# Kernel optimization log

Measured on AMD Instinct MI355X. Metric: run time of the kernel, lower is better.

## Reference

```python
import jax, jax.numpy as jnp
import numpy as np

NUM_HEADS = 16
HEAD_DIM = 64
HIDDEN = NUM_HEADS * HEAD_DIM


def _rotate_half(x):
    half = x.shape[-1] // 2
    x1, x2 = x[..., :half], x[..., half:]
    return jnp.concatenate([-x2, x1], axis=-1)


def setup_inputs() -> dict:
    key = jax.random.key(0)
    k1, k2, k3, k4, k5 = jax.random.split(key, 5)
    B, T = 2, 2048
    x = jax.random.normal(k1, (B, T, HIDDEN), dtype=jnp.float32)
    # rotary tables (seq_len, head_dim) as in apply_rope docstring
    cos = jax.random.uniform(k2, (T, HEAD_DIM), dtype=jnp.float32)
    sin = jax.random.uniform(k3, (T, HEAD_DIM), dtype=jnp.float32)
    # nn.Linear weights: y = x @ W.T ; scaled for stable fp32 activations
    w_qkv = jax.random.normal(k4, (3 * HIDDEN, HIDDEN), dtype=jnp.float32) * (1.0 / np.sqrt(HIDDEN))
    w_out = jax.random.normal(k5, (HIDDEN, HIDDEN), dtype=jnp.float32) * (1.0 / np.sqrt(HIDDEN))
    return {"x": x, "cos": cos, "sin": sin, "w_qkv": w_qkv, "w_out": w_out}


def reference(x, cos, sin, w_qkv, w_out):
    B, T, C = x.shape
    H, D = NUM_HEADS, HEAD_DIM
    qkv = jnp.einsum("btc,fc->btf", x, w_qkv)          # (B, T, 3C)
    q, k, v = jnp.split(qkv, 3, axis=-1)
    # (B, T, C) -> (B, H, T, D)
    to_heads = lambda t: t.reshape(B, T, H, D).transpose(0, 2, 1, 3)
    q, k, v = to_heads(q), to_heads(k), to_heads(v)
    # RoPE: broadcast cos/sin (T, D) over batch and heads
    cos_b = cos[None, None, :, :]
    sin_b = sin[None, None, :, :]
    q = q * cos_b + _rotate_half(q) * sin_b
    k = k * cos_b + _rotate_half(k) * sin_b
    # causal scaled dot-product attention (dropout_p = 0 in eval)
    scale = 1.0 / np.sqrt(D)
    scores = jnp.einsum("bhqd,bhkd->bhqk", q, k) * scale  # (B, H, T, T)
    causal = jnp.tril(jnp.ones((T, T), dtype=bool))
    scores = jnp.where(causal[None, None], scores, jnp.finfo(scores.dtype).min)
    probs = jax.nn.softmax(scores, axis=-1)
    out = jnp.einsum("bhqk,bhkd->bhqd", probs, v)          # (B, H, T, D)
    out = out.transpose(0, 2, 1, 3).reshape(B, T, C)
    return jnp.einsum("btc,fc->btf", out, w_out)
```

## Files before the change

kernel.cpp:

```cpp
#include <hip/hip_runtime.h>

typedef unsigned short u16;
typedef __bf16 bf16x8 __attribute__((ext_vector_type(8)));
typedef __bf16 bf16x4 __attribute__((ext_vector_type(4)));
typedef float f32x4 __attribute__((ext_vector_type(4)));

__device__ __forceinline__ u16 f2bf(float f) {
    union { float f; unsigned int i; } v; v.f = f;
    unsigned int x = v.i;
    x += 0x7fffu + ((x >> 16) & 1u);
    return (u16)(x >> 16);
}

__device__ __forceinline__ void gl_lds16(const u16* g, u16* l) {
    __builtin_amdgcn_global_load_lds(
        (const __attribute__((address_space(1))) void*)g,
        (__attribute__((address_space(3))) void*)l, 16, 0, 0);
}

__global__ __launch_bounds__(256, 2)
void cvt_xw_kernel(const float* __restrict__ X, const float* __restrict__ Wq,
                   u16* __restrict__ Xb, u16* __restrict__ Wqb)
{
    const int n1 = 4194304 / 4;
    const int n2 = 3145728 / 4;
    int i = blockIdx.x * 256 + threadIdx.x;
    const int stride = gridDim.x * 256;
    for (; i < n1 + n2; i += stride) {
        float4 v;
        ushort4* dst;
        if (i < n1) { v = ((const float4*)X)[i];       dst = (ushort4*)Xb + i; }
        else        { v = ((const float4*)Wq)[i - n1]; dst = (ushort4*)Wqb + (i - n1); }
        ushort4 o;
        o.x = f2bf(v.x); o.y = f2bf(v.y); o.z = f2bf(v.z); o.w = f2bf(v.w);
        *dst = o;
    }
}

__global__ __launch_bounds__(256, 2)
void cvt_w_kernel(const float* __restrict__ W, u16* __restrict__ Wb)
{
    int i = blockIdx.x * 256 + threadIdx.x;
    float4 v = ((const float4*)W)[i];
    ushort4 o;
    o.x = f2bf(v.x); o.y = f2bf(v.y); o.z = f2bf(v.z); o.w = f2bf(v.w);
    ((ushort4*)Wb)[i] = o;
}

__global__ __launch_bounds__(256, 2)
void qkv_rope_kernel(const u16* __restrict__ X, const u16* __restrict__ W,
                     const float* __restrict__ Cos, const float* __restrict__ Sin,
                     u16* __restrict__ Qo, u16* __restrict__ Ko, u16* __restrict__ Vo)
{
    __shared__ __align__(16) u16 As[128 * 64];
    __shared__ __align__(16) u16 Bs[128 * 64];
    const int tid  = threadIdx.x;
    const int lane = tid & 63, wave = tid >> 6;
    const int l15  = lane & 15, q4 = lane >> 4;
    const int wm = (wave >> 1) * 64, wn = (wave & 1) * 64;
    const int m0 = blockIdx.y * 128, n0 = blockIdx.x * 128;
    const int srow = lane >> 3;
    const int scol = ((lane & 7) ^ srow) * 8;

    f32x4 acc[4][4];
    #pragma unroll
    for (int i = 0; i < 4; i++)
        #pragma unroll
        for (int j = 0; j < 4; j++) { f32x4 z = {}; acc[i][j] = z; }

    for (int k0 = 0; k0 < 1024; k0 += 64) {
        __syncthreads();
        #pragma unroll
        for (int i = 0; i < 4; i++) {
            int rb = wave * 32 + i * 8;
            gl_lds16(X + (size_t)(m0 + rb + srow) * 1024 + k0 + scol, As + rb * 64);
            gl_lds16(W + (size_t)(n0 + rb + srow) * 1024 + k0 + scol, Bs + rb * 64);
        }
        __syncthreads();
        #pragma unroll
        for (int ks = 0; ks < 2; ks++) {
            const int ch = (((4 * ks + q4) ^ (l15 & 7)) * 8);
            bf16x8 af[4], bfr[4];
            #pragma unroll
            for (int i = 0; i < 4; i++) {
                af[i]  = *(const bf16x8*)&As[(wm + i * 16 + l15) * 64 + ch];
                bfr[i] = *(const bf16x8*)&Bs[(wn + i * 16 + l15) * 64 + ch];
            }
            #pragma unroll
            for (int mi = 0; mi < 4; mi++)
                #pragma unroll
                for (int ni = 0; ni < 4; ni++)
                    acc[mi][ni] = __builtin_amdgcn_mfma_f32_16x16x32_bf16(
                        af[mi], bfr[ni], acc[mi][ni], 0, 0, 0);
        }
    }

    if (n0 >= 2048) {
        #pragma unroll
        for (int mi = 0; mi < 4; mi++) {
            int t0row = m0 + wm + mi * 16 + q4 * 4;
            int b = t0row >> 11, t0 = t0row & 2047;
            #pragma unroll
            for (int ni = 0; ni < 4; ni++) {
                int col = n0 + wn + ni * 16 + l15;
                int hh  = (col >> 6) & 15;
                int d   = col & 63;
                ushort4 pk;
                pk.x = f2bf(acc[mi][ni][0]); pk.y = f2bf(acc[mi][ni][1]);
                pk.z = f2bf(acc[mi][ni][2]); pk.w = f2bf(acc[mi][ni][3]);
                *(ushort4*)&Vo[(((size_t)(b * 16 + hh)) * 64 + d) * 2048 + t0] = pk;
            }
        }
    } else {
        #pragma unroll
        for (int mi = 0; mi < 4; mi++) {
            #pragma unroll
            for (int r = 0; r < 4; r++) {
                int row = m0 + wm + mi * 16 + q4 * 4 + r;
                int b = row >> 11, t = row & 2047;
                #pragma unroll
                for (int ni = 0; ni < 4; ni++) {
                    int col = n0 + wn + ni * 16 + l15;
                    float v = acc[mi][ni][r];
                    int sec = col >> 10;
                    int hh  = (col >> 6) & 15;
                    int d   = col & 63;
                    float cs = Cos[t * 64 + d];
                    float sn = Sin[t * 64 + d];
                    float partner = acc[mi][ni ^ 2][r];
                    float rot = (d < 32) ? -partner : partner;
                    v = v * cs + rot * sn;
                    u16* dst = (sec == 0) ? Qo : Ko;
                    dst[(((size_t)(b * 16 + hh)) * 2048 + t) * 64 + d] = f2bf(v);
                }
            }
        }
    }
}

__global__ __launch_bounds__(256, 3)
void attn_kernel(const u16* __restrict__ Q, const u16* __restrict__ Kg,
                 const u16* __restrict__ Vt, u16* __restrict__ Oh)
{
    __shared__ __align__(16) u16 Ks[128 * 64];
    __shared__ __align__(16) u16 Vs[64 * 128];
    __shared__ __align__(16) __bf16 Ps[4][16][136];

    const int bx = blockIdx.x;
    const int xcd = bx & 7;
    const int i8  = bx >> 3;
    const int bh  = xcd * 4 + (i8 & 3);
    const int qt  = 31 - (i8 >> 2);
    const int b = bh >> 4, h = bh & 15;
    const int tid = threadIdx.x, wave = tid >> 6, lane = tid & 63;
    const int l15 = lane & 15, q4 = lane >> 4;
    const int srow = lane >> 3;
    const int sKcol = ((lane & 7) ^ srow) * 8;

    const size_t head_off = (size_t)bh * 2048 * 64;
    const u16* Qb = Q  + head_off;
    const u16* Kb = Kg + head_off;
    const u16* Vb = Vt + head_off;

    const int qrow0 = qt * 64 + wave * 16;

    bf16x8 qf[2];
    #pragma unroll
    for (int ks = 0; ks < 2; ks++) {
        bf16x8 t = *(const bf16x8*)(Qb + (size_t)(qrow0 + l15) * 64 + ks * 32 + q4 * 8);
        #pragma unroll
        for (int j = 0; j < 8; j++) t[j] = (__bf16)((float)t[j] * 0.125f);
        qf[ks] = t;
    }

    bf16x8 ones;
    #pragma unroll
    for (int j = 0; j < 8; j++) ones[j] = (__bf16)1.0f;

    f32x4 o[4];
    f32x4 ol = {};
    float mstq = -1e30f;
    #pragma unroll
    for (int ni = 0; ni < 4; ni++) { f32x4 z = {}; o[ni] = z; }

    const int nkv = (qt >> 1) + 1;
    for (int it = 0; it < nkv; it++) {
        const int k0 = it * 128;
        __syncthreads();
        #pragma unroll
        for (int i = 0; i < 8; i++) {
            int id = wave * 8 + i;
            if (id < 16) {
                int rb = id * 8;
                gl_lds16(Kb + (size_t)(k0 + rb + srow) * 64 + sKcol, Ks + rb * 64);
            } else {
                int rb = (id - 16) * 4;
                int d  = rb + (lane >> 4);
                int cl = ((lane & 15) ^ (d & 15)) * 8;
                gl_lds16(Vb + (size_t)d * 2048 + k0 + cl, Vs + rb * 128);
            }
        }
        __syncthreads();

        f32x4 st[2][4];
        #pragma unroll
        for (int hf = 0; hf < 2; hf++)
            #pragma unroll
            for (int mi = 0; mi < 4; mi++) { f32x4 z = {}; st[hf][mi] = z; }
        #pragma unroll
        for (int ks = 0; ks < 2; ks++) {
            const int ch = (((4 * ks + q4) ^ (l15 & 7)) * 8);
            #pragma unroll
            for (int hf = 0; hf < 2; hf++) {
                bf16x8 kf[4];
                #pragma unroll
                for (int mi = 0; mi < 4; mi++)
                    kf[mi] = *(const bf16x8*)&Ks[(hf * 64 + mi * 16 + l15) * 64 + ch];
                #pragma unroll
                for (int mi = 0; mi < 4; mi++)
                    st[hf][mi] = __builtin_amdgcn_mfma_f32_16x16x32_bf16(
                        kf[mi], qf[ks], st[hf][mi], 0, 0, 0);
            }
        }

        float rm = -1e30f;
        if (it == nkv - 1) {
            const int tq = qrow0 + l15;
            #pragma unroll
            for (int hf = 0; hf < 2; hf++)
                #pragma unroll
                for (int mi = 0; mi < 4; mi++)
                    #pragma unroll
                    for (int r = 0; r < 4; r++) {
                        float v = st[hf][mi][r];
                        if (k0 + hf * 64 + mi * 16 + q4 * 4 + r > tq) v = -1e30f;
                        st[hf][mi][r] = v;
                        rm = fmaxf(rm, v);
                    }
        } else {
            #pragma unroll
            for (int hf = 0; hf < 2; hf++)
                #pragma unroll
                for (int mi = 0; mi < 4; mi++)
                    #pragma unroll
                    for (int r = 0; r < 4; r++)
                        rm = fmaxf(rm, st[hf][mi][r]);
        }
        rm = fmaxf(rm, __shfl_xor(rm, 16, 64));
        rm = fmaxf(rm, __shfl_xor(rm, 32, 64));

        float mnew  = fmaxf(mstq, rm);
        float alpha = __expf(mstq - mnew);
        mstq = mnew;

        #pragma unroll
        for (int hf = 0; hf < 2; hf++)
            #pragma unroll
            for (int mi = 0; mi < 4; mi++) {
                bf16x4 p4;
                #pragma unroll
                for (int r = 0; r < 4; r++)
                    p4[r] = (__bf16)__expf(st[hf][mi][r] - mnew);
                *(bf16x4*)&Ps[wave][l15][hf * 64 + mi * 16 + q4 * 4] = p4;
            }

        float ar[4];
        #pragma unroll
        for (int r = 0; r < 4; r++)
            ar[r] = __shfl(alpha, q4 * 4 + r, 64);
        #pragma unroll
        for (int ni = 0; ni < 4; ni++)
            #pragma unroll
            for (int r = 0; r < 4; r++)
                o[ni][r] *= ar[r];
        #pragma unroll
        for (int r = 0; r < 4; r++)
            ol[r] *= ar[r];

        #pragma unroll
        for (int ks = 0; ks < 4; ks++) {
            bf16x8 pa = *(const bf16x8*)&Ps[wave][l15][ks * 32 + q4 * 8];
            bf16x8 vf[4];
            #pragma unroll
            for (int ni = 0; ni < 4; ni++) {
                const int pc = (((ks * 4 + q4) ^ l15) * 8);
                vf[ni] = *(const bf16x8*)&Vs[(ni * 16 + l15) * 128 + pc];
            }
            #pragma unroll
            for (int ni = 0; ni < 4; ni++)
                o[ni] = __builtin_amdgcn_mfma_f32_16x16x32_bf16(pa, vf[ni], o[ni], 0, 0, 0);
            ol = __builtin_amdgcn_mfma_f32_16x16x32_bf16(pa, ones, ol, 0, 0, 0);
        }
    }

    #pragma unroll
    for (int r = 0; r < 4; r++) {
        int t = qrow0 + q4 * 4 + r;
        float inv = 1.0f / ol[r];
        #pragma unroll
        for (int ni = 0; ni < 4; ni++) {
            int d = ni * 16 + l15;
            Oh[(((size_t)(b * 2048 + t)) * 16 + h) * 64 + d] = f2bf(o[ni][r] * inv);
        }
    }
}

__global__ __launch_bounds__(256, 4)
void outproj_kernel(const u16* __restrict__ A, const u16* __restrict__ W,
                    float* __restrict__ Cout)
{
    __shared__ __align__(16) u16 As[64 * 128];
    __shared__ __align__(16) u16 Bs[64 * 128];
    const int tid  = threadIdx.x;
    const int lane = tid & 63, wave = tid >> 6;
    const int l15  = lane & 15, q4 = lane >> 4;
    const int wm = (wave >> 1) * 32, wn = (wave & 1) * 32;
    const int m0 = blockIdx.y * 64, n0 = blockIdx.x * 64;

    f32x4 acc[2][2];
    #pragma unroll
    for (int i = 0; i < 2; i++)
        #pragma unroll
        for (int j = 0; j < 2; j++) { f32x4 z = {}; acc[i][j] = z; }

    for (int k0 = 0; k0 < 1024; k0 += 128) {
        __syncthreads();
        #pragma unroll
        for (int i = 0; i < 8; i++) {
            int id = wave * 8 + i;
            int rb = (id & 15) * 4;
            int row = rb + (lane >> 4);
            int cl  = ((lane & 15) ^ (row & 15)) * 8;
            if (id < 16)
                gl_lds16(A + (size_t)(m0 + row) * 1024 + k0 + cl, As + rb * 128);
            else
                gl_lds16(W + (size_t)(n0 + row) * 1024 + k0 + cl, Bs + rb * 128);
        }
        __syncthreads();
        #pragma unroll
        for (int ks = 0; ks < 4; ks++) {
            const int ch = (((ks * 4 + q4) ^ l15) * 8);
            bf16x8 af[2], bfr[2];
            #pragma unroll
            for (int i = 0; i < 2; i++) {
                af[i]  = *(const bf16x8*)&As[(wm + i * 16 + l15) * 128 + ch];
                bfr[i] = *(const bf16x8*)&Bs[(wn + i * 16 + l15) * 128 + ch];
            }
            #pragma unroll
            for (int mi = 0; mi < 2; mi++)
                #pragma unroll
                for (int ni = 0; ni < 2; ni++)
                    acc[mi][ni] = __builtin_amdgcn_mfma_f32_16x16x32_bf16(
                        af[mi], bfr[ni], acc[mi][ni], 0, 0, 0);
        }
    }

    #pragma unroll
    for (int mi = 0; mi < 2; mi++)
        #pragma unroll
        for (int r = 0; r < 4; r++) {
            int row = m0 + wm + mi * 16 + q4 * 4 + r;
            #pragma unroll
            for (int ni = 0; ni < 2; ni++) {
                int col = n0 + wn + ni * 16 + l15;
                Cout[(size_t)row * 1024 + col] = acc[mi][ni][r];
            }
        }
}

extern "C" void kernel_launch(void* const* d_in, const int* in_sizes, int n_in,
                              void* d_out, int out_size, void* d_ws, size_t ws_size,
                              hipStream_t stream) {
    (void)in_sizes; (void)n_in; (void)out_size; (void)ws_size;
    const float* x     = (const float*)d_in[0];
    const float* cosp  = (const float*)d_in[1];
    const float* sinp  = (const float*)d_in[2];
    const float* w_qkv = (const float*)d_in[3];
    const float* w_out = (const float*)d_in[4];
    float* out = (float*)d_out;

    const size_t NELEM = (size_t)2 * 2048 * 1024;
    u16* Q   = (u16*)d_out;
    u16* Xb  = (u16*)d_out + NELEM;
    u16* K   = (u16*)d_ws;
    u16* Vt  = K + NELEM;
    u16* Oh  = Vt + NELEM;
    u16* Wqb = Oh;
    u16* Wob = K;

    cvt_xw_kernel<<<7168, 256, 0, stream>>>(x, w_qkv, Xb, Wqb);
    qkv_rope_kernel<<<dim3(24, 32), 256, 0, stream>>>(Xb, Wqb, cosp, sinp, Q, K, Vt);
    attn_kernel<<<1024, 256, 0, stream>>>(Q, K, Vt, Oh);
    cvt_w_kernel<<<1024, 256, 0, stream>>>(w_out, Wob);
    outproj_kernel<<<dim3(16, 64), 256, 0, stream>>>(Oh, Wob, out);
}
```

Before: 178.3 us.

## Overlap V tile load with QK compute, use exp2 softmax, fuse weight conversion

Splits the K/V LDS staging so V tiles load asynchronously while QK^T is computed, adding a barrier before the PV stage. Folds log2(e) into the Q scale so softmax uses exp2. When the workspace is large enough, converts w_out in the initial conversion kernel, which removes a separate launch. These cut load latency and launch overhead at the cost of an extra barrier and a workspace-dependent code path.

```diff
diff --git a/kernel.cpp b/kernel.cpp
--- a/kernel.cpp
+++ b/kernel.cpp
@@ -19,18 +19,21 @@
 }
 
 __global__ __launch_bounds__(256, 2)
-void cvt_xw_kernel(const float* __restrict__ X, const float* __restrict__ Wq,
-                   u16* __restrict__ Xb, u16* __restrict__ Wqb)
+void cvt_all_kernel(const float* __restrict__ X, const float* __restrict__ Wq,
+                    const float* __restrict__ Wo,
+                    u16* __restrict__ Xb, u16* __restrict__ Wqb,
+                    u16* __restrict__ Wob, int n3)
 {
     const int n1 = 4194304 / 4;
     const int n2 = 3145728 / 4;
     int i = blockIdx.x * 256 + threadIdx.x;
     const int stride = gridDim.x * 256;
-    for (; i < n1 + n2; i += stride) {
+    for (; i < n1 + n2 + n3; i += stride) {
         float4 v;
         ushort4* dst;
-        if (i < n1) { v = ((const float4*)X)[i];       dst = (ushort4*)Xb + i; }
-        else        { v = ((const float4*)Wq)[i - n1]; dst = (ushort4*)Wqb + (i - n1); }
+        if (i < n1)           { v = ((const float4*)X)[i];            dst = (ushort4*)Xb  + i; }
+        else if (i < n1 + n2) { v = ((const float4*)Wq)[i - n1];      dst = (ushort4*)Wqb + (i - n1); }
+        else                  { v = ((const float4*)Wo)[i - n1 - n2]; dst = (ushort4*)Wob + (i - n1 - n2); }
         ushort4 o;
         o.x = f2bf(v.x); o.y = f2bf(v.y); o.z = f2bf(v.z); o.w = f2bf(v.w);
         *dst = o;
@@ -164,12 +167,13 @@
 
     const int qrow0 = qt * 64 + wave * 16;
 
+    const float QSCALE = 0.18033688f;
     bf16x8 qf[2];
     #pragma unroll
     for (int ks = 0; ks < 2; ks++) {
         bf16x8 t = *(const bf16x8*)(Qb + (size_t)(qrow0 + l15) * 64 + ks * 32 + q4 * 8);
         #pragma unroll
-        for (int j = 0; j < 8; j++) t[j] = (__bf16)((float)t[j] * 0.125f);
+        for (int j = 0; j < 8; j++) t[j] = (__bf16)((float)t[j] * QSCALE);
         qf[ks] = t;
     }
 
@@ -188,19 +192,18 @@
         const int k0 = it * 128;
         __syncthreads();
         #pragma unroll
-        for (int i = 0; i < 8; i++) {
-            int id = wave * 8 + i;
-            if (id < 16) {
-                int rb = id * 8;
-                gl_lds16(Kb + (size_t)(k0 + rb + srow) * 64 + sKcol, Ks + rb * 64);
-            } else {
-                int rb = (id - 16) * 4;
-                int d  = rb + (lane >> 4);
-                int cl = ((lane & 15) ^ (d & 15)) * 8;
-                gl_lds16(Vb + (size_t)d * 2048 + k0 + cl, Vs + rb * 128);
-            }
-        }
-        __syncthreads();
+        for (int i = 0; i < 4; i++) {
+            int rb = (wave * 4 + i) * 8;
+            gl_lds16(Kb + (size_t)(k0 + rb + srow) * 64 + sKcol, Ks + rb * 64);
+        }
+        __syncthreads();
+        #pragma unroll
+        for (int i = 0; i < 4; i++) {
+            int rb = (wave * 4 + i) * 4;
+            int d  = rb + (lane >> 4);
+            int cl = ((lane & 15) ^ (d & 15)) * 8;
+            gl_lds16(Vb + (size_t)d * 2048 + k0 + cl, Vs + rb * 128);
+        }
 
         f32x4 st[2][4];
         #pragma unroll
@@ -250,7 +253,7 @@
         rm = fmaxf(rm, __shfl_xor(rm, 32, 64));
 
         float mnew  = fmaxf(mstq, rm);
-        float alpha = __expf(mstq - mnew);
+        float alpha = exp2f(mstq - mnew);
         mstq = mnew;
 
         #pragma unroll
@@ -260,7 +263,7 @@
                 bf16x4 p4;
                 #pragma unroll
                 for (int r = 0; r < 4; r++)
-                    p4[r] = (__bf16)__expf(st[hf][mi][r] - mnew);
+                    p4[r] = (__bf16)exp2f(st[hf][mi][r] - mnew);
                 *(bf16x4*)&Ps[wave][l15][hf * 64 + mi * 16 + q4 * 4] = p4;
             }
 
@@ -276,6 +279,8 @@
         #pragma unroll
         for (int r = 0; r < 4; r++)
             ol[r] *= ar[r];
+
+        __syncthreads();
 
         #pragma unroll
         for (int ks = 0; ks < 4; ks++) {
@@ -371,7 +376,7 @@
 extern "C" void kernel_launch(void* const* d_in, const int* in_sizes, int n_in,
                               void* d_out, int out_size, void* d_ws, size_t ws_size,
                               hipStream_t stream) {
-    (void)in_sizes; (void)n_in; (void)out_size; (void)ws_size;
+    (void)in_sizes; (void)n_in; (void)out_size;
     const float* x     = (const float*)d_in[0];
     const float* cosp  = (const float*)d_in[1];
     const float* sinp  = (const float*)d_in[2];
@@ -386,11 +391,21 @@
     u16* Vt  = K + NELEM;
     u16* Oh  = Vt + NELEM;
     u16* Wqb = Oh;
-    u16* Wob = K;
-
-    cvt_xw_kernel<<<7168, 256, 0, stream>>>(x, w_qkv, Xb, Wqb);
-    qkv_rope_kernel<<<dim3(24, 32), 256, 0, stream>>>(Xb, Wqb, cosp, sinp, Q, K, Vt);
-    attn_kernel<<<1024, 256, 0, stream>>>(Q, K, Vt, Oh);
-    cvt_w_kernel<<<1024, 256, 0, stream>>>(w_out, Wob);
-    outproj_kernel<<<dim3(16, 64), 256, 0, stream>>>(Oh, Wob, out);
-}
+
+    const bool big = ws_size >= (24u * 1024 * 1024 + 2u * 1024 * 1024);
+    if (big) {
+        u16* Wob = K + 3 * NELEM;
+        cvt_all_kernel<<<7168, 256, 0, stream>>>(x, w_qkv, w_out, Xb, Wqb, Wob,
+                                                 262144);
+        qkv_rope_kernel<<<dim3(24, 32), 256, 0, stream>>>(Xb, Wqb, cosp, sinp, Q, K, Vt);
+        attn_kernel<<<1024, 256, 0, stream>>>(Q, K, Vt, Oh);
+        outproj_kernel<<<dim3(16, 64), 256, 0, stream>>>(Oh, Wob, out);
+    } else {
+        u16* Wob = K;
+        cvt_all_kernel<<<7168, 256, 0, stream>>>(x, w_qkv, w_out, Xb, Wqb, Wob, 0);
+        qkv_rope_kernel<<<dim3(24, 32), 256, 0, stream>>>(Xb, Wqb, cosp, sinp, Q, K, Vt);
+        attn_kernel<<<1024, 256, 0, stream>>>(Q, K, Vt, Oh);
+        cvt_w_kernel<<<1024, 256, 0, stream>>>(w_out, Wob);
+        outproj_kernel<<<dim3(16, 64), 256, 0, stream>>>(Oh, Wob, out);
+    }
+}
```

Result: faster. 172.4 us (-3.3%).
